# Kernel tuning notes

Hardware: AMD Instinct MI355X
Metric: run time of the kernel (lower is better)

Reference implementation:

```python
import jax, jax.numpy as jnp
import numpy as np

E = 1024   # embed_dim
H = 16     # num_heads
D = E // H # head_dim = 64
HD2 = D // 2
B = 2
S = 2048


def setup_inputs() -> dict:
    key = jax.random.key(0)
    ks = jax.random.split(key, 12)
    def lin(k, fan_in, fan_out):
        # xavier-uniform-ish init, stored in [in, out] (jax) convention
        lim = float(np.sqrt(6.0 / (fan_in + fan_out)))
        return jax.random.uniform(k, (fan_in, fan_out), jnp.float32, -lim, lim)
    return {
        "query": jax.random.normal(ks[0], (B, S, E), jnp.float32),
        "xi_scale": jax.random.uniform(ks[1], (B,), jnp.float32),
        "Wq": lin(ks[2], E, E), "bq": jnp.zeros((E,), jnp.float32),
        "Wk": lin(ks[3], E, E), "bk": jnp.zeros((E,), jnp.float32),
        "Wv": lin(ks[4], E, E), "bv": jnp.zeros((E,), jnp.float32),
        "Wo": lin(ks[5], E, E), "bo": jnp.zeros((E,), jnp.float32),
        "enc_w1": lin(ks[6], 1, HD2), "enc_b1": jnp.zeros((HD2,), jnp.float32),
        "ln_g": jnp.ones((HD2,), jnp.float32), "ln_b": jnp.zeros((HD2,), jnp.float32),
        "enc_w2": lin(ks[7], HD2, D), "enc_b2": jnp.zeros((D,), jnp.float32),
        "scale_gating": jnp.ones((H,), jnp.float32),
    }


def reference(query, xi_scale, Wq, bq, Wk, bk, Wv, bv, Wo, bo,
              enc_w1, enc_b1, ln_g, ln_b, enc_w2, enc_b2, scale_gating):
    b, s, e = query.shape
    h, d = H, e // H
    # --- scale adaptation: xi -> Linear -> LayerNorm -> GELU -> Linear ---
    x = xi_scale[:, None] @ enc_w1 + enc_b1                  # [B, D/2]
    mu = x.mean(-1, keepdims=True)
    var = ((x - mu) ** 2).mean(-1, keepdims=True)
    x = (x - mu) / jnp.sqrt(var + 1e-5) * ln_g + ln_b
    x = jax.nn.gelu(x, approximate=False)
    xe = x @ enc_w2 + enc_b2                                 # [B, D]
    adapt = 1.0 + jax.nn.sigmoid(scale_gating)[None, :, None] * xe[:, None, :]  # [B, H, D]
    # --- projections (self-attention: key = value = query) ---
    q = (query @ Wq + bq).reshape(b, s, h, d).transpose(0, 2, 1, 3) * adapt[:, :, None, :]
    k = (query @ Wk + bk).reshape(b, s, h, d).transpose(0, 2, 1, 3) * adapt[:, :, None, :]
    v = (query @ Wv + bv).reshape(b, s, h, d).transpose(0, 2, 1, 3)
    # --- explicit QK^T / sqrt(d) -> softmax -> V ---
    inv_scale = 1.0 / float(np.sqrt(d))
    scores = jnp.einsum('bhqd,bhkd->bhqk', q, k) * inv_scale  # [B, H, S, S]
    attn = jax.nn.softmax(scores, axis=-1)
    out = jnp.einsum('bhqk,bhkd->bhqd', attn, v)              # [B, H, S, D]
    out = out.transpose(0, 2, 1, 3).reshape(b, s, e)
    return out @ Wo + bo
```

## Files before the change

### kernel.cpp

```cpp
#include <hip/hip_runtime.h>

typedef __bf16 bf16;
typedef __attribute__((ext_vector_type(8))) __bf16 bf16x8;
typedef __attribute__((ext_vector_type(4))) float f32x4;
typedef unsigned int u32;

#define MFMA16(a, b, c) __builtin_amdgcn_mfma_f32_16x16x32_bf16((a), (b), (c), 0, 0, 0)

#define BB 2
#define SS 2048
#define EE 1024
#define HH 16
#define DD 64
#define MM (BB * SS)

#define TM 128
#define TN 64
#define BK 64

__device__ inline f32x4 zero4() {
    f32x4 z; z.x = 0.f; z.y = 0.f; z.z = 0.f; z.w = 0.f; return z;
}

__device__ __forceinline__ void gload16(const bf16* g, bf16* l) {
    __builtin_amdgcn_global_load_lds(
        (const __attribute__((address_space(1))) u32*)(const void*)g,
        (__attribute__((address_space(3))) u32*)(void*)l,
        16, 0, 0);
}

__global__ __launch_bounds__(256) void prep_kernel(
    const float* __restrict__ query, bf16* __restrict__ qc,
    const float* __restrict__ s0, const float* __restrict__ s1,
    const float* __restrict__ s2, const float* __restrict__ s3,
    bf16* __restrict__ d0, bf16* __restrict__ d1,
    bf16* __restrict__ d2, bf16* __restrict__ d3,
    const float* __restrict__ xi, const float* __restrict__ w1,
    const float* __restrict__ b1, const float* __restrict__ lng,
    const float* __restrict__ lnb, const float* __restrict__ w2,
    const float* __restrict__ b2, const float* __restrict__ gate,
    float* __restrict__ adapt) {
    __shared__ bf16 tile[64 * 72];
    const int bid = blockIdx.x;
    const int t = threadIdx.x;

    if (bid < 2048) {
        const int i = (bid * 256 + t) * 8;
        float4 a = *(const float4*)(query + i);
        float4 b = *(const float4*)(query + i + 4);
        bf16 tmp[8];
        tmp[0] = (bf16)a.x; tmp[1] = (bf16)a.y; tmp[2] = (bf16)a.z; tmp[3] = (bf16)a.w;
        tmp[4] = (bf16)b.x; tmp[5] = (bf16)b.y; tmp[6] = (bf16)b.z; tmp[7] = (bf16)b.w;
        *(uint4*)(qc + i) = *(uint4*)tmp;
    } else if (bid < 3072) {
        const int m = (bid - 2048) >> 8;
        const int idx0 = (bid - 2048) & 255;
        const float* W = (m == 0) ? s0 : (m == 1) ? s1 : (m == 2) ? s2 : s3;
        bf16* Wt = (m == 0) ? d0 : (m == 1) ? d1 : (m == 2) ? d2 : d3;
        const int k0 = (idx0 >> 4) * 64, n0 = (idx0 & 15) * 64;
#pragma unroll
        for (int i = 0; i < 2; ++i) {
            int idx = i * 256 + t;
            int r = idx >> 3, c = (idx & 7) * 8;
            float4 a = *(const float4*)(W + (k0 + r) * EE + n0 + c);
            float4 b = *(const float4*)(W + (k0 + r) * EE + n0 + c + 4);
            bf16 tmp[8];
            tmp[0] = (bf16)a.x; tmp[1] = (bf16)a.y; tmp[2] = (bf16)a.z; tmp[3] = (bf16)a.w;
            tmp[4] = (bf16)b.x; tmp[5] = (bf16)b.y; tmp[6] = (bf16)b.z; tmp[7] = (bf16)b.w;
            *(uint4*)(tile + r * 72 + c) = *(uint4*)tmp;
        }
        __syncthreads();
#pragma unroll
        for (int i = 0; i < 2; ++i) {
            int idx = i * 256 + t;
            int n = idx >> 3, kc = (idx & 7) * 8;
            bf16 tmp[8];
#pragma unroll
            for (int j = 0; j < 8; ++j) tmp[j] = tile[(kc + j) * 72 + n];
            *(uint4*)(Wt + (n0 + n) * EE + k0 + kc) = *(uint4*)tmp;
        }
    } else {
        const int b = bid - 3072;
        float* xs = (float*)tile;
        if (t < 64) {
            const float xiv = xi[b];
            float xv = 0.f;
            if (t < 32) xv = xiv * w1[t] + b1[t];
            float sm = xv;
            for (int off = 1; off < 32; off <<= 1) sm += __shfl_xor(sm, off);
            const float mu = sm * (1.f / 32.f);
            float dv = (t < 32) ? (xv - mu) : 0.f;
            float s2 = dv * dv;
            for (int off = 1; off < 32; off <<= 1) s2 += __shfl_xor(s2, off);
            const float var = s2 * (1.f / 32.f);
            if (t < 32) {
                float xn = (xv - mu) * rsqrtf(var + 1e-5f) * lng[t] + lnb[t];
                float ge = 0.5f * xn * (1.f + erff(xn * 0.70710678118654752f));
                xs[t] = ge;
            }
        }
        __syncthreads();
        if (t < 64) {
            float acc = b2[t];
            for (int j = 0; j < 32; ++j) acc += xs[j] * w2[j * DD + t];
            for (int h = 0; h < HH; ++h) {
                float sg = 1.f / (1.f + __expf(-gate[h]));
                adapt[(b * HH + h) * DD + t] = 1.f + sg * acc;
            }
        }
    }
}

__global__ __launch_bounds__(256, 3) void gemm_epi(
    const bf16* __restrict__ Aq, const bf16* __restrict__ Bqk,
    const bf16* __restrict__ Av,
    const float* __restrict__ bias, const float* __restrict__ bias2,
    const float* __restrict__ bias3, const float* __restrict__ adapt,
    bf16* __restrict__ outqk, bf16* __restrict__ outvt,
    float* __restrict__ outf, int mode) {
    __shared__ bf16 As[2 * TM * BK];
    __shared__ bf16 Bs[2 * TN * BK];

    const int t = threadIdx.x;
    const int w = t >> 6, lane = t & 63;
    const int mrow = lane & 15, quad = lane >> 4;

    int md = mode, bx, by;
    const bf16 *Ap, *Bp;
    if (mode == 6) {
        int bid = blockIdx.x;
        if (bid < 1024) { md = 5; bx = bid & 31; by = bid >> 5; Ap = Aq; Bp = Bqk; }
        else { md = 4; bid -= 1024; bx = bid & 7; by = bid >> 3; Ap = Av; Bp = Aq; }
    } else {
        bx = blockIdx.x; by = blockIdx.y; Ap = Aq; Bp = Bqk;
    }
    const int m0 = bx * TM, n0 = by * TN;

    f32x4 acc[2][4];
#pragma unroll
    for (int i = 0; i < 2; ++i)
#pragma unroll
        for (int j = 0; j < 4; ++j) acc[i][j] = zero4();

    const int grow = lane >> 3;
    const int gsw = ((lane & 7) ^ grow) * 8;
    const bf16* Ag = Ap + (size_t)(m0 + w * 32 + grow) * EE + gsw;
    const bf16* Bg = Bp + (size_t)(n0 + w * 16 + grow) * EE + gsw;
    bf16* Al = As + (w * 32) * BK;
    bf16* Bl = Bs + (w * 16) * BK;

#pragma unroll
    for (int i = 0; i < 4; ++i) gload16(Ag + i * 8 * EE, Al + i * 8 * BK);
#pragma unroll
    for (int i = 0; i < 2; ++i) gload16(Bg + i * 8 * EE, Bl + i * 8 * BK);

    for (int kt = 0; kt < EE / BK; ++kt) {
        __syncthreads();
        if (kt < EE / BK - 1) {
            const int kn = (kt + 1) * BK;
            const int nb = (kt + 1) & 1;
#pragma unroll
            for (int i = 0; i < 4; ++i)
                gload16(Ag + i * 8 * EE + kn, Al + nb * TM * BK + i * 8 * BK);
#pragma unroll
            for (int i = 0; i < 2; ++i)
                gload16(Bg + i * 8 * EE + kn, Bl + nb * TN * BK + i * 8 * BK);
        }
        const bf16* Ab = As + (kt & 1) * TM * BK;
        const bf16* Bb = Bs + (kt & 1) * TN * BK;
#pragma unroll
        for (int ks = 0; ks < 2; ++ks) {
            const int cg = ks * 4 + quad;
            const int sw = (cg ^ (mrow & 7)) * 8;
            bf16x8 af[2], bfr[4];
#pragma unroll
            for (int mi = 0; mi < 2; ++mi)
                af[mi] = *(const bf16x8*)(Ab + (w * 32 + mi * 16 + mrow) * BK + sw);
#pragma unroll
            for (int nj = 0; nj < 4; ++nj)
                bfr[nj] = *(const bf16x8*)(Bb + (nj * 16 + mrow) * BK + sw);
#pragma unroll
            for (int mi = 0; mi < 2; ++mi)
#pragma unroll
                for (int nj = 0; nj < 4; ++nj)
                    acc[mi][nj] = MFMA16(af[mi], bfr[nj], acc[mi][nj]);
        }
    }

#pragma unroll
    for (int mi = 0; mi < 2; ++mi) {
#pragma unroll
        for (int nj = 0; nj < 4; ++nj) {
            const int col = n0 + nj * 16 + mrow;
#pragma unroll
            for (int r = 0; r < 4; ++r) {
                const int row = m0 + w * 32 + mi * 16 + quad * 4 + r;
                float v = acc[mi][nj][r];
                if (md == 3) {
                    outf[row * EE + col] = v + bias[col];
                } else if (md == 4) {
                    v += bias3[row];
                    const int h = row >> 6, d = row & 63;
                    const int b = col >> 11, s = col & (SS - 1);
                    outvt[(((b * HH + h) * DD + d) * SS) + s] = (bf16)v;
                } else {
                    const int m2 = col >> 10;
                    const int cl = col & 1023;
                    const int h = cl >> 6, d = cl & 63;
                    const int b = row >> 11, s = row & (SS - 1);
                    v += (m2 ? bias2[cl] : bias[cl]);
                    v *= adapt[(b * HH + h) * DD + d];
                    if (!m2) v *= 0.125f;
                    outqk[(size_t)m2 * MM * EE + ((b * HH + h) * SS + s) * DD + d] = (bf16)v;
                }
            }
        }
    }
}

__global__ __launch_bounds__(256, 2) void attn_kernel(
    const bf16* __restrict__ q, const bf16* __restrict__ k,
    const bf16* __restrict__ vt, bf16* __restrict__ o0, bf16* __restrict__ o1,
    float* __restrict__ lws) {
    __shared__ bf16 Ks[64 * 72];
    __shared__ bf16 Vt[64 * 72];
    __shared__ bf16 Ps[4][32 * 72];

    const int t = threadIdx.x;
    const int wave = t >> 6, lane = t & 63;
    const int mrow = lane & 15, quad = lane >> 4;
    const int split = blockIdx.x >> 9;
    const int rest = blockIdx.x & 511;
    const int bh = rest >> 4;
    const int qb = rest & 15;

    const int qr0 = qb * 128 + wave * 32;
    bf16x8 qf[2][2];
#pragma unroll
    for (int m = 0; m < 2; ++m)
#pragma unroll
        for (int h = 0; h < 2; ++h)
            qf[m][h] = *(const bf16x8*)(q + (bh * SS + qr0 + m * 16 + mrow) * DD +
                                        h * 32 + quad * 8);

    f32x4 oacc[2][4];
    float lst[2][4];
#pragma unroll
    for (int m = 0; m < 2; ++m) {
#pragma unroll
        for (int jd = 0; jd < 4; ++jd) oacc[m][jd] = zero4();
#pragma unroll
        for (int r = 0; r < 4; ++r) lst[m][r] = 0.f;
    }

    const int sr = t >> 2;
    const int sc = (t & 3) * 16;
    const bf16* kg = k + (size_t)(bh * SS) * DD;
    const bf16* vg = vt + (size_t)(bh * DD + sr) * SS;

    const int ktbeg = split * (SS / 128), ktend = ktbeg + (SS / 128);

    uint4 kreg0 = *(const uint4*)(kg + (ktbeg * 64 + sr) * DD + sc);
    uint4 kreg1 = *(const uint4*)(kg + (ktbeg * 64 + sr) * DD + sc + 8);
    uint4 vreg0 = *(const uint4*)(vg + ktbeg * 64 + sc);
    uint4 vreg1 = *(const uint4*)(vg + ktbeg * 64 + sc + 8);

    for (int kt = ktbeg; kt < ktend; ++kt) {
        __syncthreads();
        *(uint4*)(Ks + sr * 72 + sc) = kreg0;
        *(uint4*)(Ks + sr * 72 + sc + 8) = kreg1;
        *(uint4*)(Vt + sr * 72 + sc) = vreg0;
        *(uint4*)(Vt + sr * 72 + sc + 8) = vreg1;
        __syncthreads();

        if (kt < ktend - 1) {
            const int kn = (kt + 1) * 64;
            kreg0 = *(const uint4*)(kg + (kn + sr) * DD + sc);
            kreg1 = *(const uint4*)(kg + (kn + sr) * DD + sc + 8);
            vreg0 = *(const uint4*)(vg + kn + sc);
            vreg1 = *(const uint4*)(vg + kn + sc + 8);
        }

        f32x4 sv[2][4];
#pragma unroll
        for (int j = 0; j < 4; ++j) {
            bf16x8 kf0 = *(const bf16x8*)(Ks + (j * 16 + mrow) * 72 + quad * 8);
            bf16x8 kf1 = *(const bf16x8*)(Ks + (j * 16 + mrow) * 72 + 32 + quad * 8);
#pragma unroll
            for (int m = 0; m < 2; ++m) {
                f32x4 z = zero4();
                z = MFMA16(qf[m][0], kf0, z);
                z = MFMA16(qf[m][1], kf1, z);
                sv[m][j] = z;
            }
        }

#pragma unroll
        for (int m = 0; m < 2; ++m)
#pragma unroll
            for (int j = 0; j < 4; ++j)
#pragma unroll
                for (int r = 0; r < 4; ++r) {
                    float p = __expf(sv[m][j][r]);
                    lst[m][r] += p;
                    Ps[wave][(m * 16 + quad * 4 + r) * 72 + j * 16 + mrow] = (bf16)p;
                }

        bf16x8 pf[2][2];
#pragma unroll
        for (int m = 0; m < 2; ++m)
#pragma unroll
            for (int c = 0; c < 2; ++c)
                pf[m][c] = *(const bf16x8*)(&Ps[wave][(m * 16 + mrow) * 72 +
                                                      c * 32 + quad * 8]);
#pragma unroll
        for (int jd = 0; jd < 4; ++jd) {
#pragma unroll
            for (int c = 0; c < 2; ++c) {
                bf16x8 vf = *(const bf16x8*)(Vt + (jd * 16 + mrow) * 72 +
                                             c * 32 + quad * 8);
#pragma unroll
                for (int m = 0; m < 2; ++m)
                    oacc[m][jd] = MFMA16(pf[m][c], vf, oacc[m][jd]);
            }
        }
    }

#pragma unroll
    for (int m = 0; m < 2; ++m)
        for (int off = 1; off < 16; off <<= 1) {
#pragma unroll
            for (int r = 0; r < 4; ++r) lst[m][r] += __shfl_xor(lst[m][r], off);
        }

    bf16* op = split ? o1 : o0;
    const int b = bh >> 4, h = bh & 15;
#pragma unroll
    for (int m = 0; m < 2; ++m) {
#pragma unroll
        for (int jd = 0; jd < 4; ++jd) {
#pragma unroll
            for (int r = 0; r < 4; ++r) {
                int row = qr0 + m * 16 + quad * 4 + r;
                op[(b * SS + row) * EE + h * DD + jd * 16 + mrow] = (bf16)oacc[m][jd][r];
            }
        }
    }
    if (mrow == 0) {
#pragma unroll
        for (int m = 0; m < 2; ++m)
#pragma unroll
            for (int r = 0; r < 4; ++r)
                lws[split * (32 * SS) + bh * SS + qr0 + m * 16 + quad * 4 + r] = lst[m][r];
    }
}

__global__ __launch_bounds__(256) void combine_kernel(
    const bf16* __restrict__ p1, const float* __restrict__ lws,
    bf16* __restrict__ o) {
    const int i = (blockIdx.x * 256 + threadIdx.x) * 8;
    const int b = i >> 21, s = (i >> 10) & (SS - 1), h = (i >> 6) & 15;
    const int li = (b * HH + h) * SS + s;
    const float inv = 1.f / (lws[li] + lws[32 * SS + li]);
    uint4 u0 = *(const uint4*)(o + i);
    uint4 u1 = *(const uint4*)(p1 + i);
    bf16 a0[8], a1[8], res[8];
    *(uint4*)a0 = u0; *(uint4*)a1 = u1;
#pragma unroll
    for (int j = 0; j < 8; ++j) res[j] = (bf16)(((float)a0[j] + (float)a1[j]) * inv);
    *(uint4*)(o + i) = *(uint4*)res;
}

extern "C" void kernel_launch(void* const* d_in, const int* in_sizes, int n_in,
                              void* d_out, int out_size, void* d_ws, size_t ws_size,
                              hipStream_t stream) {
    const float* query = (const float*)d_in[0];
    const float* xi    = (const float*)d_in[1];
    const float* Wq = (const float*)d_in[2];  const float* bq = (const float*)d_in[3];
    const float* Wk = (const float*)d_in[4];  const float* bk = (const float*)d_in[5];
    const float* Wv = (const float*)d_in[6];  const float* bv = (const float*)d_in[7];
    const float* Wo = (const float*)d_in[8];  const float* bo = (const float*)d_in[9];
    const float* ew1 = (const float*)d_in[10]; const float* eb1 = (const float*)d_in[11];
    const float* lng = (const float*)d_in[12]; const float* lnb = (const float*)d_in[13];
    const float* ew2 = (const float*)d_in[14]; const float* eb2 = (const float*)d_in[15];
    const float* gate = (const float*)d_in[16];
    float* out = (float*)d_out;

    char* ws = (char*)d_ws;
    const size_t SZ = (size_t)MM * EE * sizeof(bf16);
    bf16* queryc = (bf16*)(ws);
    bf16* p0     = (bf16*)(ws);
    bf16* qws    = (bf16*)(ws + SZ);
    bf16* kws    = (bf16*)(ws + 2 * SZ);
    bf16* wqT    = (bf16*)(ws + 3 * SZ);
    bf16* wkT    = (bf16*)(ws + 3 * SZ + 2097152);
    bf16* wvT    = (bf16*)(ws + 3 * SZ + 2 * 2097152);
    bf16* woT    = (bf16*)(ws + 3 * SZ + 3 * 2097152);
    float* adaptws = (float*)(ws + 4 * SZ);
    float* lws   = (float*)(ws + 4 * SZ + 8192);
    bf16* vtws   = (bf16*)d_out;
    bf16* p1     = (bf16*)((char*)d_out + SZ);

    prep_kernel<<<3074, 256, 0, stream>>>(query, queryc, Wq, Wk, Wv, Wo,
                                          wqT, wkT, wvT, woT,
                                          xi, ew1, eb1, lng, lnb, ew2, eb2, gate,
                                          adaptws);

    gemm_epi<<<1536, 256, 0, stream>>>(queryc, wqT, wvT, bq, bk, bv, adaptws,
                                       qws, vtws, nullptr, 6);

    attn_kernel<<<2 * BB * HH * (SS / 128), 256, 0, stream>>>(qws, kws, vtws, p0, p1, lws);
    combine_kernel<<<MM * EE / (256 * 8), 256, 0, stream>>>(p1, lws, p0);

    gemm_epi<<<dim3(MM / TM, EE / TN), 256, 0, stream>>>(
        p0, woT, nullptr, bo, nullptr, nullptr, nullptr, nullptr, nullptr, out, 3);
}
```

Baseline: 234.0 us.

## Rewrite attention inner loop with 32x32 MFMA, register-resident P and async LDS loads

The attention kernel moves from 16x16x32 to 32x32x16 bf16 MFMAs and computes S^T = K·Q so the probabilities stay in registers. A lane-xor-32 shuffle rearranges them into the operand layout for the PV product instead of going through an LDS round trip. K and V tiles are double-buffered in XOR-swizzled LDS and filled with global_load_lds direct loads, which drops the register staging and one barrier per iteration. Output goes through LDS for coalesced 16-byte stores, and the occupancy hint is raised to 3 blocks per CU. Risks are correctness of the shuffle and swizzle layout, and register pressure from the larger accumulators.

Measured after the change: 230.9 us. No clear change (-1.3%).

```diff
diff --git a/kernel.cpp b/kernel.cpp
--- a/kernel.cpp
+++ b/kernel.cpp
@@ -3,9 +3,11 @@
 typedef __bf16 bf16;
 typedef __attribute__((ext_vector_type(8))) __bf16 bf16x8;
 typedef __attribute__((ext_vector_type(4))) float f32x4;
+typedef __attribute__((ext_vector_type(16))) float f32x16;
 typedef unsigned int u32;
 
 #define MFMA16(a, b, c) __builtin_amdgcn_mfma_f32_16x16x32_bf16((a), (b), (c), 0, 0, 0)
+#define MFMA32(a, b, c) __builtin_amdgcn_mfma_f32_32x32x16_bf16((a), (b), (c), 0, 0, 0)
 
 #define BB 2
 #define SS 2048
@@ -27,6 +29,12 @@
         (const __attribute__((address_space(1))) u32*)(const void*)g,
         (__attribute__((address_space(3))) u32*)(void*)l,
         16, 0, 0);
+}
+
+__device__ __forceinline__ u32 pkbf(float a, float b) {
+    union { __bf16 h; unsigned short s; } ua, ub;
+    ua.h = (__bf16)a; ub.h = (__bf16)b;
+    return (u32)ua.s | ((u32)ub.s << 16);
 }
 
 __global__ __launch_bounds__(256) void prep_kernel(
@@ -218,141 +226,139 @@
     }
 }
 
-__global__ __launch_bounds__(256, 2) void attn_kernel(
+__global__ __launch_bounds__(256, 3) void attn_kernel(
     const bf16* __restrict__ q, const bf16* __restrict__ k,
     const bf16* __restrict__ vt, bf16* __restrict__ o0, bf16* __restrict__ o1,
     float* __restrict__ lws) {
-    __shared__ bf16 Ks[64 * 72];
-    __shared__ bf16 Vt[64 * 72];
-    __shared__ bf16 Ps[4][32 * 72];
+    __shared__ bf16 lds[16384];
+    bf16* Ks = lds;
+    bf16* Vs = lds + 8192;
 
     const int t = threadIdx.x;
-    const int wave = t >> 6, lane = t & 63;
-    const int mrow = lane & 15, quad = lane >> 4;
+    const int w = t >> 6, lane = t & 63;
+    const int q32 = lane & 31, h = lane >> 5;
     const int split = blockIdx.x >> 9;
     const int rest = blockIdx.x & 511;
     const int bh = rest >> 4;
     const int qb = rest & 15;
-
-    const int qr0 = qb * 128 + wave * 32;
-    bf16x8 qf[2][2];
-#pragma unroll
-    for (int m = 0; m < 2; ++m)
-#pragma unroll
-        for (int h = 0; h < 2; ++h)
-            qf[m][h] = *(const bf16x8*)(q + (bh * SS + qr0 + m * 16 + mrow) * DD +
-                                        h * 32 + quad * 8);
-
-    f32x4 oacc[2][4];
-    float lst[2][4];
-#pragma unroll
-    for (int m = 0; m < 2; ++m) {
-#pragma unroll
-        for (int jd = 0; jd < 4; ++jd) oacc[m][jd] = zero4();
-#pragma unroll
-        for (int r = 0; r < 4; ++r) lst[m][r] = 0.f;
-    }
-
-    const int sr = t >> 2;
-    const int sc = (t & 3) * 16;
-    const bf16* kg = k + (size_t)(bh * SS) * DD;
-    const bf16* vg = vt + (size_t)(bh * DD + sr) * SS;
+    const int qr0 = qb * 128 + w * 32;
+
+    bf16x8 qf[4];
+#pragma unroll
+    for (int c = 0; c < 4; ++c)
+        qf[c] = *(const bf16x8*)(q + (size_t)(bh * SS + qr0 + q32) * DD + c * 16 + h * 8);
+
+    f32x16 oacc[2];
+#pragma unroll
+    for (int mf = 0; mf < 2; ++mf)
+#pragma unroll
+        for (int i = 0; i < 16; ++i) oacc[mf][i] = 0.f;
+    float lsum = 0.f;
+
+    const int dr = lane >> 3;
+    const int dcg = ((lane & 7) ^ dr) * 8;
+    const bf16* kg = k + (size_t)bh * SS * DD;
+    const bf16* vg = vt + (size_t)bh * DD * SS;
+    const bf16* kgl = kg + (size_t)dr * DD + dcg;
+    const bf16* vgl = vg + (size_t)(w * 16 + dr) * SS + dcg;
 
     const int ktbeg = split * (SS / 128), ktend = ktbeg + (SS / 128);
 
-    uint4 kreg0 = *(const uint4*)(kg + (ktbeg * 64 + sr) * DD + sc);
-    uint4 kreg1 = *(const uint4*)(kg + (ktbeg * 64 + sr) * DD + sc + 8);
-    uint4 vreg0 = *(const uint4*)(vg + ktbeg * 64 + sc);
-    uint4 vreg1 = *(const uint4*)(vg + ktbeg * 64 + sc + 8);
+#pragma unroll
+    for (int i = 0; i < 2; ++i) {
+        const int rb = w * 16 + i * 8;
+        gload16(kgl + (size_t)(ktbeg * 64 + rb) * DD, Ks + rb * 64);
+        gload16(vgl + (size_t)(i * 8) * SS + ktbeg * 64, Vs + rb * 64);
+    }
 
     for (int kt = ktbeg; kt < ktend; ++kt) {
         __syncthreads();
-        *(uint4*)(Ks + sr * 72 + sc) = kreg0;
-        *(uint4*)(Ks + sr * 72 + sc + 8) = kreg1;
-        *(uint4*)(Vt + sr * 72 + sc) = vreg0;
-        *(uint4*)(Vt + sr * 72 + sc + 8) = vreg1;
-        __syncthreads();
-
         if (kt < ktend - 1) {
-            const int kn = (kt + 1) * 64;
-            kreg0 = *(const uint4*)(kg + (kn + sr) * DD + sc);
-            kreg1 = *(const uint4*)(kg + (kn + sr) * DD + sc + 8);
-            vreg0 = *(const uint4*)(vg + kn + sc);
-            vreg1 = *(const uint4*)(vg + kn + sc + 8);
-        }
-
-        f32x4 sv[2][4];
-#pragma unroll
-        for (int j = 0; j < 4; ++j) {
-            bf16x8 kf0 = *(const bf16x8*)(Ks + (j * 16 + mrow) * 72 + quad * 8);
-            bf16x8 kf1 = *(const bf16x8*)(Ks + (j * 16 + mrow) * 72 + 32 + quad * 8);
-#pragma unroll
-            for (int m = 0; m < 2; ++m) {
-                f32x4 z = zero4();
-                z = MFMA16(qf[m][0], kf0, z);
-                z = MFMA16(qf[m][1], kf1, z);
-                sv[m][j] = z;
-            }
-        }
-
-#pragma unroll
-        for (int m = 0; m < 2; ++m)
-#pragma unroll
-            for (int j = 0; j < 4; ++j)
-#pragma unroll
-                for (int r = 0; r < 4; ++r) {
-                    float p = __expf(sv[m][j][r]);
-                    lst[m][r] += p;
-                    Ps[wave][(m * 16 + quad * 4 + r) * 72 + j * 16 + mrow] = (bf16)p;
-                }
-
-        bf16x8 pf[2][2];
-#pragma unroll
-        for (int m = 0; m < 2; ++m)
-#pragma unroll
-            for (int c = 0; c < 2; ++c)
-                pf[m][c] = *(const bf16x8*)(&Ps[wave][(m * 16 + mrow) * 72 +
-                                                      c * 32 + quad * 8]);
-#pragma unroll
-        for (int jd = 0; jd < 4; ++jd) {
-#pragma unroll
-            for (int c = 0; c < 2; ++c) {
-                bf16x8 vf = *(const bf16x8*)(Vt + (jd * 16 + mrow) * 72 +
-                                             c * 32 + quad * 8);
-#pragma unroll
-                for (int m = 0; m < 2; ++m)
-                    oacc[m][jd] = MFMA16(pf[m][c], vf, oacc[m][jd]);
-            }
-        }
-    }
-
-#pragma unroll
-    for (int m = 0; m < 2; ++m)
-        for (int off = 1; off < 16; off <<= 1) {
-#pragma unroll
-            for (int r = 0; r < 4; ++r) lst[m][r] += __shfl_xor(lst[m][r], off);
-        }
+            const int nb = (kt + 1) & 1;
+#pragma unroll
+            for (int i = 0; i < 2; ++i) {
+                const int rb = w * 16 + i * 8;
+                gload16(kgl + (size_t)((kt + 1) * 64 + rb) * DD, Ks + nb * 4096 + rb * 64);
+                gload16(vgl + (size_t)(i * 8) * SS + (kt + 1) * 64, Vs + nb * 4096 + rb * 64);
+            }
+        }
+        const bf16* Kb = Ks + (kt & 1) * 4096;
+        const bf16* Vb = Vs + (kt & 1) * 4096;
+
+        f32x16 st[2];
+#pragma unroll
+        for (int mf = 0; mf < 2; ++mf)
+#pragma unroll
+            for (int i = 0; i < 16; ++i) st[mf][i] = 0.f;
+#pragma unroll
+        for (int c = 0; c < 4; ++c) {
+            const int sw = ((2 * c + h) ^ (q32 & 7)) * 8;
+#pragma unroll
+            for (int mf = 0; mf < 2; ++mf) {
+                bf16x8 kf = *(const bf16x8*)(Kb + (mf * 32 + q32) * 64 + sw);
+                st[mf] = MFMA32(kf, qf[c], st[mf]);
+            }
+        }
+
+        u32 P32[2][8];
+#pragma unroll
+        for (int mf = 0; mf < 2; ++mf)
+#pragma unroll
+            for (int rp = 0; rp < 8; ++rp) {
+                float pa = __expf(st[mf][2 * rp]);
+                float pb = __expf(st[mf][2 * rp + 1]);
+                lsum += pa + pb;
+                P32[mf][rp] = pkbf(pa, pb);
+            }
+
+#pragma unroll
+        for (int c = 0; c < 4; ++c) {
+            const int mfs = c >> 1;
+            const int ro = (c & 1) * 4;
+            u32 vA0 = P32[mfs][ro + 0], vA1 = P32[mfs][ro + 1];
+            u32 vB0 = P32[mfs][ro + 2], vB1 = P32[mfs][ro + 3];
+            u32 prep0 = h ? vA0 : vB0;
+            u32 prep1 = h ? vA1 : vB1;
+            u32 sh0 = __shfl_xor(prep0, 32);
+            u32 sh1 = __shfl_xor(prep1, 32);
+            union { u32 u[4]; bf16x8 v; } pb;
+            pb.u[0] = h ? sh0 : vA0;
+            pb.u[1] = h ? sh1 : vA1;
+            pb.u[2] = h ? vB0 : sh0;
+            pb.u[3] = h ? vB1 : sh1;
+            const int sw = ((2 * c + h) ^ (q32 & 7)) * 8;
+#pragma unroll
+            for (int mf = 0; mf < 2; ++mf) {
+                bf16x8 vf = *(const bf16x8*)(Vb + (mf * 32 + q32) * 64 + sw);
+                oacc[mf] = MFMA32(vf, pb.v, oacc[mf]);
+            }
+        }
+    }
+
+    lsum += __shfl_xor(lsum, 32);
+
+    __syncthreads();
+    bf16* ob = lds + w * 2112;
+#pragma unroll
+    for (int mf = 0; mf < 2; ++mf)
+#pragma unroll
+        for (int rp = 0; rp < 8; ++rp) {
+            const int d = 32 * mf + 2 * (rp & 1) + 8 * (rp >> 1) + 4 * h;
+            *(u32*)(ob + q32 * 66 + d) = pkbf(oacc[mf][2 * rp], oacc[mf][2 * rp + 1]);
+        }
+    __builtin_amdgcn_s_waitcnt(0);
 
     bf16* op = split ? o1 : o0;
-    const int b = bh >> 4, h = bh & 15;
-#pragma unroll
-    for (int m = 0; m < 2; ++m) {
-#pragma unroll
-        for (int jd = 0; jd < 4; ++jd) {
-#pragma unroll
-            for (int r = 0; r < 4; ++r) {
-                int row = qr0 + m * 16 + quad * 4 + r;
-                op[(b * SS + row) * EE + h * DD + jd * 16 + mrow] = (bf16)oacc[m][jd][r];
-            }
-        }
-    }
-    if (mrow == 0) {
-#pragma unroll
-        for (int m = 0; m < 2; ++m)
-#pragma unroll
-            for (int r = 0; r < 4; ++r)
-                lws[split * (32 * SS) + bh * SS + qr0 + m * 16 + quad * 4 + r] = lst[m][r];
-    }
+    const int b = bh >> 4, head = bh & 15;
+    const int qq = lane >> 1, half = lane & 1;
+#pragma unroll
+    for (int i = 0; i < 4; ++i) {
+        bf16x8 val = *(const bf16x8*)(ob + qq * 66 + half * 32 + i * 8);
+        *(bf16x8*)(op + (size_t)(b * SS + qr0 + qq) * EE + head * DD +
+                   half * 32 + i * 8) = val;
+    }
+    if (lane < 32)
+        lws[split * (32 * SS) + bh * SS + qr0 + q32] = lsum;
 }
 
 __global__ __launch_bounds__(256) void combine_kernel(
```
